# Optimization experiments

Hardware: AMD Instinct MI355X
Metric: run time of the kernel (lower is better)

Reference implementation:

```python
import jax, jax.numpy as jnp
import numpy as np

D_MODEL = 1024
N_HEADS = 16
D_HEAD = D_MODEL // N_HEADS  # 64
D_FF = D_MODEL  # FeedForward(d_model, d_model) in source
B, S = 4, 1024
EPS = 1e-5


def layer_norm(x, gamma, beta):
    mu = jnp.mean(x, axis=-1, keepdims=True)
    var = jnp.mean(jnp.square(x - mu), axis=-1, keepdims=True)
    return (x - mu) * jax.lax.rsqrt(var + EPS) * gamma + beta


def setup_inputs() -> dict:
    key = jax.random.key(0)
    ks = jax.random.split(key, 16)
    s_embed = 1.0 / np.sqrt(D_MODEL)
    s_ff = 1.0 / np.sqrt(D_FF)
    return {
        "x": jax.random.normal(ks[0], (B, S, D_MODEL), jnp.float32),
        # per-head QKV projections stacked over heads: [H, d_embed, d_head]
        "Wq": jax.random.normal(ks[1], (N_HEADS, D_MODEL, D_HEAD), jnp.float32) * s_embed,
        "bq": jax.random.normal(ks[2], (N_HEADS, D_HEAD), jnp.float32) * s_embed,
        "Wk": jax.random.normal(ks[3], (N_HEADS, D_MODEL, D_HEAD), jnp.float32) * s_embed,
        "bk": jax.random.normal(ks[4], (N_HEADS, D_HEAD), jnp.float32) * s_embed,
        "Wv": jax.random.normal(ks[5], (N_HEADS, D_MODEL, D_HEAD), jnp.float32) * s_embed,
        "bv": jax.random.normal(ks[6], (N_HEADS, D_HEAD), jnp.float32) * s_embed,
        "Wo": jax.random.normal(ks[7], (D_MODEL, D_MODEL), jnp.float32) * s_embed,
        "bo": jax.random.normal(ks[8], (D_MODEL,), jnp.float32) * s_embed,
        "g1": jnp.ones((D_MODEL,), jnp.float32),
        "be1": jnp.zeros((D_MODEL,), jnp.float32),
        "W1": jax.random.normal(ks[9], (D_MODEL, D_FF), jnp.float32) * s_embed,
        "b1": jax.random.normal(ks[10], (D_FF,), jnp.float32) * s_embed,
        "W2": jax.random.normal(ks[11], (D_FF, D_MODEL), jnp.float32) * s_ff,
        "b2": jax.random.normal(ks[12], (D_MODEL,), jnp.float32) * s_ff,
        "g2": jnp.ones((D_MODEL,), jnp.float32),
        "be2": jnp.zeros((D_MODEL,), jnp.float32),
    }


def reference(x, Wq, bq, Wk, bk, Wv, bv, Wo, bo, g1, be1, W1, b1, W2, b2, g2, be2):
    scale = 1.0 / np.sqrt(D_HEAD).astype(np.float32)
    # batched per-head projections (equivalent to the per-head Linear loop)
    Q = jnp.einsum('bse,hed->bhsd', x, Wq) + bq[None, :, None, :]
    K = jnp.einsum('bse,hed->bhsd', x, Wk) + bk[None, :, None, :]
    V = jnp.einsum('bse,hed->bhsd', x, Wv) + bv[None, :, None, :]
    scores = jnp.einsum('bhsd,bhtd->bhst', Q, K) * scale
    attn = jax.nn.softmax(scores, axis=-1)
    ctx = jnp.einsum('bhst,bhtd->bhsd', attn, V)
    # concat heads along feature dim (head order matches the torch cat)
    ctx = jnp.transpose(ctx, (0, 2, 1, 3)).reshape(x.shape[0], x.shape[1], D_MODEL)
    attn_out = ctx @ Wo + bo
    y1 = layer_norm(x + attn_out, g1, be1)
    ff = jax.nn.relu(y1 @ W1 + b1) @ W2 + b2  # dropout is identity in eval
    return layer_norm(y1 + ff, g2, be2)
```

## Files before the change

kernel.cpp:

```cpp
#include <hip/hip_runtime.h>
#include <stdint.h>

#define BSZ 4
#define SEQ 1024
#define DM 1024
#define NH 16
#define DH 64
#define ROWS (BSZ * SEQ)
#define QS3 3072

typedef unsigned short u16;
typedef short bf16x8 __attribute__((ext_vector_type(8)));
typedef float f32x4 __attribute__((ext_vector_type(4)));

__device__ __forceinline__ float b2f(u16 u) {
    union { uint32_t i; float f; } v; v.i = ((uint32_t)u) << 16; return v.f;
}
__device__ __forceinline__ u16 f2b(float f) {
    union { float f; uint32_t i; } v; v.f = f;
    uint32_t u = v.i;
    return (u16)((u + 0x7FFFu + ((u >> 16) & 1u)) >> 16);
}
__device__ __forceinline__ u16 f2b_rh(float f) {
    union { float f; uint32_t i; } v; v.f = f;
    return (u16)((v.i + 0x8000u) >> 16);
}

typedef const __attribute__((address_space(1))) void gv_t;
typedef __attribute__((address_space(3))) void lv_t;
__device__ __forceinline__ void gl_lds16(const void* g, void* l) {
    __builtin_amdgcn_global_load_lds((gv_t*)g, (lv_t*)l, 16, 0, 0);
}

__global__ __launch_bounds__(256) void detect_dtype(
    const uint32_t* __restrict__ x, int* __restrict__ flag)
{
    __shared__ int red[256];
    const int tid = threadIdx.x;
    int sane = 0;
    for (int i = tid; i < 1024; i += 256) {
        uint32_t w = x[i];
        uint32_t lo = w & 0xFFFFu;
        uint32_t e = (lo >> 7) & 0xFF;
        if ((e >= 100 && e <= 140) || lo == 0) sane++;
    }
    red[tid] = sane;
    __syncthreads();
    for (int st = 128; st > 0; st >>= 1) {
        if (tid < st) red[tid] += red[tid + st];
        __syncthreads();
    }
    if (tid == 0) flag[0] = (red[0] < 512) ? 1 : 0;
}

__global__ __launch_bounds__(256) void convert_generic(
    const void* __restrict__ src, u16* __restrict__ dst, int n,
    const int* __restrict__ flag)
{
    int i = blockIdx.x * 256 + threadIdx.x;
    if (i >= n) return;
    if (flag[0]) dst[i] = f2b(((const float*)src)[i]);
    else         dst[i] = ((const u16*)src)[i];
}

__global__ __launch_bounds__(256) void convert_vecs(
    const void* bq, const void* bk, const void* bv, const void* bo,
    const void* b1, const void* b2, const void* g1, const void* be1,
    const void* g2, const void* be2, u16* __restrict__ dst,
    const int* __restrict__ flag)
{
    int i = blockIdx.x * 256 + threadIdx.x;
    int seg = i >> 10, off = i & 1023;
    const void* srcs[10] = {bq, bk, bv, bo, b1, b2, g1, be1, g2, be2};
    const void* s = srcs[seg];
    if (flag[0]) dst[i] = f2b(((const float*)s)[off]);
    else         dst[i] = ((const u16*)s)[off];
}

__global__ __launch_bounds__(256) void transpose_convert(
    const void* __restrict__ src, u16* __restrict__ dst, int R, int C,
    const int* __restrict__ flag)
{
    __shared__ u16 Ts[32][33];
    const int t = threadIdx.x;
    const int cb = blockIdx.x * 32, rb = blockIdx.y * 32, z = blockIdx.z;
    const int tr = t >> 3, tc4 = (t & 7) * 4;
    const size_t sbase = (size_t)z * R * C;

    u16 v[4];
    if (flag[0]) {
        const float* s = (const float*)src + sbase + (size_t)(rb + tr) * C + cb + tc4;
        float4 f = *(const float4*)s;
        v[0] = f2b(f.x); v[1] = f2b(f.y); v[2] = f2b(f.z); v[3] = f2b(f.w);
    } else {
        const u16* s = (const u16*)src + sbase + (size_t)(rb + tr) * C + cb + tc4;
        ushort4 f = *(const ushort4*)s;
        v[0] = f.x; v[1] = f.y; v[2] = f.z; v[3] = f.w;
    }
    #pragma unroll
    for (int j = 0; j < 4; ++j) Ts[tc4 + j][tr] = v[j];
    __syncthreads();

    u16* d = dst + (size_t)(z * C + cb + tr) * R + rb + tc4;
    ushort4 o;
    o.x = Ts[tr][tc4 + 0]; o.y = Ts[tr][tc4 + 1];
    o.z = Ts[tr][tc4 + 2]; o.w = Ts[tr][tc4 + 3];
    *(ushort4*)d = o;
}

__global__ __launch_bounds__(256) void gemm_mfma(
    const u16* __restrict__ A, const u16* __restrict__ Bt,
    const u16* __restrict__ bias, const u16* __restrict__ resid,
    u16* __restrict__ C, int M, int N, int K, int relu)
{
    __shared__ u16 As[2][128 * 32];
    __shared__ u16 Bs[2][128 * 32];
    const int tid = threadIdx.x;
    const int w = tid >> 6, lane = tid & 63;
    const int l16 = lane & 15, quad = lane >> 4;
    const int wr = w >> 1, wc = w & 1;
    const int bm = blockIdx.y * 128, bn = blockIdx.x * 128;

    f32x4 acc[4][4];
    #pragma unroll
    for (int i = 0; i < 4; ++i)
        #pragma unroll
        for (int j = 0; j < 4; ++j)
            acc[i][j] = (f32x4){0.f, 0.f, 0.f, 0.f};

    const int srow = lane >> 2, scol = (lane & 3) * 8;
    const u16* gA0 = A  + (size_t)(bm + w * 16 + srow) * K + scol;
    const u16* gA1 = gA0 + (size_t)64 * K;
    const u16* gB0 = Bt + (size_t)(bn + w * 16 + srow) * K + scol;
    const u16* gB1 = gB0 + (size_t)64 * K;
    const int lo0 = (w * 16) * 32, lo1 = (64 + w * 16) * 32;

    gl_lds16(gA0, &As[0][lo0]);
    gl_lds16(gA1, &As[0][lo1]);
    gl_lds16(gB0, &Bs[0][lo0]);
    gl_lds16(gB1, &Bs[0][lo1]);
    __syncthreads();

    const int nk = K >> 5;
    for (int kt = 0; kt < nk; ++kt) {
        const int cur = kt & 1, nxt = cur ^ 1;
        if (kt + 1 < nk) {
            const int off = (kt + 1) * 32;
            gl_lds16(gA0 + off, &As[nxt][lo0]);
            gl_lds16(gA1 + off, &As[nxt][lo1]);
            gl_lds16(gB0 + off, &Bs[nxt][lo0]);
            gl_lds16(gB1 + off, &Bs[nxt][lo1]);
        }

        bf16x8 a[4], b[4];
        #pragma unroll
        for (int i = 0; i < 4; ++i)
            a[i] = *(const bf16x8*)&As[cur][(wr * 64 + i * 16 + l16) * 32 + quad * 8];
        #pragma unroll
        for (int j = 0; j < 4; ++j)
            b[j] = *(const bf16x8*)&Bs[cur][(wc * 64 + j * 16 + l16) * 32 + quad * 8];

        #pragma unroll
        for (int i = 0; i < 4; ++i)
            #pragma unroll
            for (int j = 0; j < 4; ++j)
                acc[i][j] = __builtin_amdgcn_mfma_f32_16x16x32_bf16(a[i], b[j], acc[i][j], 0, 0, 0);
        __syncthreads();
    }

    #pragma unroll
    for (int j = 0; j < 4; ++j) {
        const int col = bn + wc * 64 + j * 16 + l16;
        const float bj = bias ? b2f(bias[col]) : 0.f;
        #pragma unroll
        for (int i = 0; i < 4; ++i) {
            const int row0 = bm + wr * 64 + i * 16 + quad * 4;
            #pragma unroll
            for (int r = 0; r < 4; ++r) {
                const int row = row0 + r;
                float v = acc[i][j][r] + bj;
                if (resid) v += b2f(resid[(size_t)row * N + col]);
                if (relu)  v = v > 0.f ? v : 0.f;
                C[(size_t)row * N + col] = f2b(v);
            }
        }
    }
}

__global__ __launch_bounds__(256) void gemm_mfma64(
    const u16* __restrict__ A, const u16* __restrict__ Bt,
    const u16* __restrict__ bias, const u16* __restrict__ resid,
    u16* __restrict__ C, int M, int N, int K, int relu)
{
    __shared__ u16 As[2][128 * 32];
    __shared__ u16 Bs[2][64 * 32];
    const int tid = threadIdx.x;
    const int w = tid >> 6, lane = tid & 63;
    const int l16 = lane & 15, quad = lane >> 4;
    const int bm = blockIdx.y * 128, bn = blockIdx.x * 64;

    f32x4 acc[2][4];
    #pragma unroll
    for (int i = 0; i < 2; ++i)
        #pragma unroll
        for (int j = 0; j < 4; ++j)
            acc[i][j] = (f32x4){0.f, 0.f, 0.f, 0.f};

    const int srow = lane >> 2, scol = (lane & 3) * 8;
    const u16* gA0 = A  + (size_t)(bm + w * 16 + srow) * K + scol;
    const u16* gA1 = gA0 + (size_t)64 * K;
    const u16* gB0 = Bt + (size_t)(bn + w * 16 + srow) * K + scol;
    const int lo0 = (w * 16) * 32, lo1 = (64 + w * 16) * 32;

    gl_lds16(gA0, &As[0][lo0]);
    gl_lds16(gA1, &As[0][lo1]);
    gl_lds16(gB0, &Bs[0][lo0]);
    __syncthreads();

    const int nk = K >> 5;
    for (int kt = 0; kt < nk; ++kt) {
        const int cur = kt & 1, nxt = cur ^ 1;
        if (kt + 1 < nk) {
            const int off = (kt + 1) * 32;
            gl_lds16(gA0 + off, &As[nxt][lo0]);
            gl_lds16(gA1 + off, &As[nxt][lo1]);
            gl_lds16(gB0 + off, &Bs[nxt][lo0]);
        }

        bf16x8 a[2], b[4];
        #pragma unroll
        for (int i = 0; i < 2; ++i)
            a[i] = *(const bf16x8*)&As[cur][(w * 32 + i * 16 + l16) * 32 + quad * 8];
        #pragma unroll
        for (int j = 0; j < 4; ++j)
            b[j] = *(const bf16x8*)&Bs[cur][(j * 16 + l16) * 32 + quad * 8];

        #pragma unroll
        for (int i = 0; i < 2; ++i)
            #pragma unroll
            for (int j = 0; j < 4; ++j)
                acc[i][j] = __builtin_amdgcn_mfma_f32_16x16x32_bf16(a[i], b[j], acc[i][j], 0, 0, 0);
        __syncthreads();
    }

    #pragma unroll
    for (int j = 0; j < 4; ++j) {
        const int col = bn + j * 16 + l16;
        const float bj = bias ? b2f(bias[col]) : 0.f;
        #pragma unroll
        for (int i = 0; i < 2; ++i) {
            const int row0 = bm + w * 32 + i * 16 + quad * 4;
            #pragma unroll
            for (int r = 0; r < 4; ++r) {
                const int row = row0 + r;
                float v = acc[i][j][r] + bj;
                if (resid) v += b2f(resid[(size_t)row * N + col]);
                if (relu)  v = v > 0.f ? v : 0.f;
                C[(size_t)row * N + col] = f2b(v);
            }
        }
    }
}

__global__ __launch_bounds__(512) void attn_mfma(
    const u16* __restrict__ QKV, u16* __restrict__ ctx)
{
    __shared__ u16 Qf[8192];
    __shared__ u16 Kf[2][4096];
    __shared__ u16 VtT[2][64 * 72];
    __shared__ u16 Ps[8 * 16 * 72];

    const int qt = blockIdx.x, h = blockIdx.y, b = blockIdx.z;
    const int tid = threadIdx.x;
    const int w = tid >> 6, lane = tid & 63;
    const int l16 = lane & 15, quad = lane >> 4;
    const size_t qrow0 = (size_t)(b * SEQ + qt * 128);
    const size_t brow = (size_t)(b * SEQ);
    const int hoff = h * DH;

    const size_t qg = (qrow0 + w * 16 + l16) * QS3 + hoff + quad * 8;
    gl_lds16(&QKV[qg],      &Qf[w * 1024]);
    gl_lds16(&QKV[qg + 32], &Qf[w * 1024 + 512]);

    const int kt_ = w >> 1, kh_ = w & 1;
    const size_t kgbase = (size_t)(kt_ * 16 + l16) * QS3 + 1024 + hoff + kh_ * 32 + quad * 8;
    const int kdst = kt_ * 1024 + kh_ * 512;

    const int vk2 = (tid & 31) * 2, vd0 = (tid >> 5) * 4;
    const size_t vgbase = (size_t)vk2 * QS3 + 2048 + hoff + vd0;

    gl_lds16(&QKV[brow * QS3 + kgbase], &Kf[0][kdst]);
    {
        uint2 a0 = *(const uint2*)&QKV[brow * QS3 + vgbase];
        uint2 a1 = *(const uint2*)&QKV[brow * QS3 + vgbase + QS3];
        uint32_t w0 = (a0.x & 0xFFFFu) | (a1.x << 16);
        uint32_t w1 = (a0.x >> 16)     | (a1.x & 0xFFFF0000u);
        uint32_t w2 = (a0.y & 0xFFFFu) | (a1.y << 16);
        uint32_t w3 = (a0.y >> 16)     | (a1.y & 0xFFFF0000u);
        *(uint32_t*)&VtT[0][(vd0 + 0) * 72 + vk2] = w0;
        *(uint32_t*)&VtT[0][(vd0 + 1) * 72 + vk2] = w1;
        *(uint32_t*)&VtT[0][(vd0 + 2) * 72 + vk2] = w2;
        *(uint32_t*)&VtT[0][(vd0 + 3) * 72 + vk2] = w3;
    }
    __syncthreads();

    bf16x8 aQ0 = *(const bf16x8*)&Qf[w * 1024 +       lane * 8];
    bf16x8 aQ1 = *(const bf16x8*)&Qf[w * 1024 + 512 + lane * 8];

    f32x4 O[4];
    #pragma unroll
    for (int dt = 0; dt < 4; ++dt) O[dt] = (f32x4){0.f, 0.f, 0.f, 0.f};
    float lacc[4] = {0.f, 0.f, 0.f, 0.f};

    for (int kt64 = 0; kt64 < SEQ / 64; ++kt64) {
        const int cur = kt64 & 1, nxt = cur ^ 1;
        uint2 a0, a1;
        const bool more = (kt64 + 1 < SEQ / 64);
        if (more) {
            const size_t krow = brow + (size_t)(kt64 + 1) * 64;
            gl_lds16(&QKV[krow * QS3 + kgbase], &Kf[nxt][kdst]);
            a0 = *(const uint2*)&QKV[krow * QS3 + vgbase];
            a1 = *(const uint2*)&QKV[krow * QS3 + vgbase + QS3];
        }

        f32x4 St[4];
        #pragma unroll
        for (int t = 0; t < 4; ++t) {
            bf16x8 b0 = *(const bf16x8*)&Kf[cur][t * 1024 +       lane * 8];
            bf16x8 b1 = *(const bf16x8*)&Kf[cur][t * 1024 + 512 + lane * 8];
            f32x4 z = (f32x4){0.f, 0.f, 0.f, 0.f};
            z = __builtin_amdgcn_mfma_f32_16x16x32_bf16(aQ0, b0, z, 0, 0, 0);
            z = __builtin_amdgcn_mfma_f32_16x16x32_bf16(aQ1, b1, z, 0, 0, 0);
            St[t] = z;
        }

        #pragma unroll
        for (int t = 0; t < 4; ++t)
            #pragma unroll
            for (int r = 0; r < 4; ++r) {
                const float p = __expf(St[t][r] * 0.125f);
                lacc[r] += p;
                Ps[w * 1152 + (quad * 4 + r) * 72 + t * 16 + l16] = f2b_rh(p);
            }

        bf16x8 aP0 = *(const bf16x8*)&Ps[w * 1152 + l16 * 72 +  0 + quad * 8];
        bf16x8 aP1 = *(const bf16x8*)&Ps[w * 1152 + l16 * 72 + 32 + quad * 8];
        #pragma unroll
        for (int dt = 0; dt < 4; ++dt) {
            bf16x8 vv0 = *(const bf16x8*)&VtT[cur][(dt * 16 + l16) * 72 +  0 + quad * 8];
            bf16x8 vv1 = *(const bf16x8*)&VtT[cur][(dt * 16 + l16) * 72 + 32 + quad * 8];
            O[dt] = __builtin_amdgcn_mfma_f32_16x16x32_bf16(aP0, vv0, O[dt], 0, 0, 0);
            O[dt] = __builtin_amdgcn_mfma_f32_16x16x32_bf16(aP1, vv1, O[dt], 0, 0, 0);
        }

        if (more) {
            uint32_t w0 = (a0.x & 0xFFFFu) | (a1.x << 16);
            uint32_t w1 = (a0.x >> 16)     | (a1.x & 0xFFFF0000u);
            uint32_t w2 = (a0.y & 0xFFFFu) | (a1.y << 16);
            uint32_t w3 = (a0.y >> 16)     | (a1.y & 0xFFFF0000u);
            *(uint32_t*)&VtT[nxt][(vd0 + 0) * 72 + vk2] = w0;
            *(uint32_t*)&VtT[nxt][(vd0 + 1) * 72 + vk2] = w1;
            *(uint32_t*)&VtT[nxt][(vd0 + 2) * 72 + vk2] = w2;
            *(uint32_t*)&VtT[nxt][(vd0 + 3) * 72 + vk2] = w3;
        }
        __syncthreads();
    }

    #pragma unroll
    for (int r = 0; r < 4; ++r) {
        float s = lacc[r];
        s += __shfl_xor(s, 1);
        s += __shfl_xor(s, 2);
        s += __shfl_xor(s, 4);
        s += __shfl_xor(s, 8);
        const float inv = 1.0f / s;
        const size_t qgr = qrow0 + w * 16 + quad * 4 + r;
        #pragma unroll
        for (int dt = 0; dt < 4; ++dt)
            ctx[qgr * DM + hoff + dt * 16 + l16] = f2b(O[dt][r] * inv);
    }
}

__global__ __launch_bounds__(256) void layernorm_kernel(
    const u16* __restrict__ X, const u16* __restrict__ gamma,
    const u16* __restrict__ beta, void* __restrict__ Y,
    const int* __restrict__ flag, int out_adaptive)
{
    __shared__ float red[256], red2[256];
    const int r = blockIdx.x, tid = threadIdx.x;
    const u16* xp = X + (size_t)r * DM;

    ushort4 v = *(const ushort4*)(xp + tid * 4);
    float x0 = b2f(v.x), x1 = b2f(v.y), x2 = b2f(v.z), x3 = b2f(v.w);
    red[tid]  = x0 + x1 + x2 + x3;
    red2[tid] = x0 * x0 + x1 * x1 + x2 * x2 + x3 * x3;
    __syncthreads();
    for (int st = 128; st > 0; st >>= 1) {
        if (tid < st) { red[tid] += red[tid + st]; red2[tid] += red2[tid + st]; }
        __syncthreads();
    }
    const float mu = red[0] * (1.0f / DM);
    const float var = red2[0] * (1.0f / DM) - mu * mu;
    const float rstd = rsqrtf(var + 1e-5f);

    ushort4 g = *(const ushort4*)(gamma + tid * 4);
    ushort4 be = *(const ushort4*)(beta + tid * 4);
    float y0 = (x0 - mu) * rstd * b2f(g.x) + b2f(be.x);
    float y1 = (x1 - mu) * rstd * b2f(g.y) + b2f(be.y);
    float y2 = (x2 - mu) * rstd * b2f(g.z) + b2f(be.z);
    float y3 = (x3 - mu) * rstd * b2f(g.w) + b2f(be.w);

    const size_t off = (size_t)r * DM + tid * 4;
    if (out_adaptive && flag[0]) {
        float* yp = (float*)Y + off;
        yp[0] = y0; yp[1] = y1; yp[2] = y2; yp[3] = y3;
    } else {
        u16* yp = (u16*)Y + off;
        yp[0] = f2b(y0); yp[1] = f2b(y1); yp[2] = f2b(y2); yp[3] = f2b(y3);
    }
}

extern "C" void kernel_launch(void* const* d_in, const int* in_sizes, int n_in,
                              void* d_out, int out_size, void* d_ws, size_t ws_size,
                              hipStream_t stream) {
    const void* x_raw   = d_in[0];
    const void* Wq_raw  = d_in[1];
    const void* bq_raw  = d_in[2];
    const void* Wk_raw  = d_in[3];
    const void* bk_raw  = d_in[4];
    const void* Wv_raw  = d_in[5];
    const void* bv_raw  = d_in[6];
    const void* Wo_raw  = d_in[7];
    const void* bo_raw  = d_in[8];
    const void* g1_raw  = d_in[9];
    const void* be1_raw = d_in[10];
    const void* W1_raw  = d_in[11];
    const void* b1_raw  = d_in[12];
    const void* W2_raw  = d_in[13];
    const void* b2_raw  = d_in[14];
    const void* g2_raw  = d_in[15];
    const void* be2_raw = d_in[16];

    char* ws = (char*)d_ws;
    const size_t MB = 1024 * 1024;
    int* flag   = (int*)ws;
    u16* x_c    = (u16*)(ws + 1 * MB);
    u16* WqkvT  = (u16*)(ws + 9 * MB);
    u16* WoT    = (u16*)(ws + 15 * MB);
    u16* W1T    = (u16*)(ws + 17 * MB);
    u16* W2T    = (u16*)(ws + 19 * MB);
    u16* vecs   = (u16*)(ws + 21 * MB);
    u16* bqkv_c = vecs;
    u16* bo_c   = vecs + 3072;
    u16* b1_c   = vecs + 4096;
    u16* b2_c   = vecs + 5120;
    u16* g1_c   = vecs + 6144;
    u16* be1_c  = vecs + 7168;
    u16* g2_c   = vecs + 8192;
    u16* be2_c  = vecs + 9216;
    u16* QKVb   = (u16*)(ws + 22 * MB);
    u16* ctx    = (u16*)(ws + 48 * MB);
    u16* res1   = (u16*)(ws + 56 * MB);
    u16* y1     = QKVb;
    u16* hmid   = QKVb + 4 * MB;
    u16* res2   = res1;

    detect_dtype<<<1, 256, 0, stream>>>((const uint32_t*)x_raw, flag);

    const int NX = ROWS * DM;
    convert_generic<<<NX / 256, 256, 0, stream>>>(x_raw, x_c, NX, flag);

    dim3 gt_qkv(DH / 32, DM / 32, NH);
    transpose_convert<<<gt_qkv, 256, 0, stream>>>(Wq_raw, WqkvT,               DM, DH, flag);
    transpose_convert<<<gt_qkv, 256, 0, stream>>>(Wk_raw, WqkvT + 1024 * 1024, DM, DH, flag);
    transpose_convert<<<gt_qkv, 256, 0, stream>>>(Wv_raw, WqkvT + 2048 * 1024, DM, DH, flag);
    dim3 gt_sq(DM / 32, DM / 32, 1);
    transpose_convert<<<gt_sq, 256, 0, stream>>>(Wo_raw, WoT, DM, DM, flag);
    transpose_convert<<<gt_sq, 256, 0, stream>>>(W1_raw, W1T, DM, DM, flag);
    transpose_convert<<<gt_sq, 256, 0, stream>>>(W2_raw, W2T, DM, DM, flag);

    convert_vecs<<<40, 256, 0, stream>>>(bq_raw, bk_raw, bv_raw, bo_raw,
                                         b1_raw, b2_raw, g1_raw, be1_raw,
                                         g2_raw, be2_raw, vecs, flag);

    gemm_mfma<<<dim3(QS3 / 128, ROWS / 128), 256, 0, stream>>>(
        x_c, WqkvT, bqkv_c, nullptr, QKVb, ROWS, QS3, DM, 0);

    attn_mfma<<<dim3(SEQ / 128, NH, BSZ), 512, 0, stream>>>(QKVb, ctx);

    dim3 gg64(DM / 64, ROWS / 128);
    gemm_mfma64<<<gg64, 256, 0, stream>>>(ctx, WoT, bo_c, x_c, res1, ROWS, DM, DM, 0);
    layernorm_kernel<<<ROWS, 256, 0, stream>>>(res1, g1_c, be1_c, (void*)y1, flag, 0);
    gemm_mfma64<<<gg64, 256, 0, stream>>>(y1, W1T, b1_c, nullptr, hmid, ROWS, DM, DM, 1);
    gemm_mfma64<<<gg64, 256, 0, stream>>>(hmid, W2T, b2_c, y1, res2, ROWS, DM, DM, 0);
    layernorm_kernel<<<ROWS, 256, 0, stream>>>(res2, g2_c, be2_c, d_out, flag, 1);
}
```

Baseline: 303.4 us.

## Store GEMM operands in pre-tiled blocked layout and stage epilogue through LDS

Introduces a blocked tile layout (128 rows x 32 k per 4096-element tile, arranged in the MFMA fragment order) for x, the transposed weights, ctx, y1 and hmid. Every producer kernel (conversion, transpose, attention, layernorm, GEMM epilogue) now writes into this layout, so the GEMM's global-to-LDS loads become fully contiguous and its LDS reads avoid bank conflicts. GEMM epilogues also stage results in LDS and write them out as 16-byte vector stores instead of scattered 2-byte stores. The cost is more complex indexing throughout, a residual read that gathers from the blocked layout, and extra LDS traffic in the epilogue.

```diff
diff --git a/kernel.cpp b/kernel.cpp
--- a/kernel.cpp
+++ b/kernel.cpp
@@ -24,6 +24,12 @@
 __device__ __forceinline__ u16 f2b_rh(float f) {
     union { float f; uint32_t i; } v; v.f = f;
     return (u16)((v.i + 0x8000u) >> 16);
+}
+
+__device__ __forceinline__ size_t blk_idx(int row, int col, int nkt) {
+    return (((size_t)((row >> 7) * nkt + (col >> 5))) << 12)
+         + ((((row >> 4) & 7) * 64 + ((col >> 3) & 3) * 16 + (row & 15)) << 3)
+         + (col & 7);
 }
 
 typedef const __attribute__((address_space(1))) void gv_t;
@@ -53,16 +59,6 @@
     if (tid == 0) flag[0] = (red[0] < 512) ? 1 : 0;
 }
 
-__global__ __launch_bounds__(256) void convert_generic(
-    const void* __restrict__ src, u16* __restrict__ dst, int n,
-    const int* __restrict__ flag)
-{
-    int i = blockIdx.x * 256 + threadIdx.x;
-    if (i >= n) return;
-    if (flag[0]) dst[i] = f2b(((const float*)src)[i]);
-    else         dst[i] = ((const u16*)src)[i];
-}
-
 __global__ __launch_bounds__(256) void convert_vecs(
     const void* bq, const void* bk, const void* bv, const void* bo,
     const void* b1, const void* b2, const void* g1, const void* be1,
@@ -77,14 +73,36 @@
     else         dst[i] = ((const u16*)s)[off];
 }
 
-__global__ __launch_bounds__(256) void transpose_convert(
+__global__ __launch_bounds__(256) void convert_x_blocked(
+    const void* __restrict__ src, u16* __restrict__ dst,
+    const int* __restrict__ flag)
+{
+    const int gid = blockIdx.x * 256 + threadIdx.x;
+    const int tile = gid >> 9, c = gid & 511;
+    const int p = tile >> 5, t = tile & 31;
+    const int r = p * 128 + ((c >> 6) & 7) * 16 + (c & 15);
+    const int k = t * 32 + ((c >> 4) & 3) * 8;
+    union { uint4 q; u16 s[8]; } o;
+    if (flag[0]) {
+        const float* s = (const float*)src + (size_t)r * DM + k;
+        float4 f0 = *(const float4*)s;
+        float4 f1 = *(const float4*)(s + 4);
+        o.s[0] = f2b(f0.x); o.s[1] = f2b(f0.y); o.s[2] = f2b(f0.z); o.s[3] = f2b(f0.w);
+        o.s[4] = f2b(f1.x); o.s[5] = f2b(f1.y); o.s[6] = f2b(f1.z); o.s[7] = f2b(f1.w);
+    } else {
+        o.q = *(const uint4*)((const u16*)src + (size_t)r * DM + k);
+    }
+    *(uint4*)&dst[(size_t)gid * 8] = o.q;
+}
+
+__global__ __launch_bounds__(256) void transpose_blocked(
     const void* __restrict__ src, u16* __restrict__ dst, int R, int C,
-    const int* __restrict__ flag)
+    int n_off, const int* __restrict__ flag)
 {
     __shared__ u16 Ts[32][33];
-    const int t = threadIdx.x;
+    const int tid = threadIdx.x;
     const int cb = blockIdx.x * 32, rb = blockIdx.y * 32, z = blockIdx.z;
-    const int tr = t >> 3, tc4 = (t & 7) * 4;
+    const int tr = tid >> 3, tc4 = (tid & 7) * 4;
     const size_t sbase = (size_t)z * R * C;
 
     u16 v[4];
@@ -101,25 +119,37 @@
     for (int j = 0; j < 4; ++j) Ts[tc4 + j][tr] = v[j];
     __syncthreads();
 
-    u16* d = dst + (size_t)(z * C + cb + tr) * R + rb + tc4;
-    ushort4 o;
-    o.x = Ts[tr][tc4 + 0]; o.y = Ts[tr][tc4 + 1];
-    o.z = Ts[tr][tc4 + 2]; o.w = Ts[tr][tc4 + 3];
-    *(ushort4*)d = o;
-}
-
-__global__ __launch_bounds__(256) void gemm_mfma(
-    const u16* __restrict__ A, const u16* __restrict__ Bt,
+    if (tid < 128) {
+        const int np = tid & 31, qp = tid >> 5;
+        const int n = n_off + z * C + cb + np;
+        const int k = rb + qp * 8;
+        union { uint4 q; u16 s[8]; } o;
+        #pragma unroll
+        for (int j = 0; j < 8; ++j) o.s[j] = Ts[np][qp * 8 + j];
+        *(uint4*)&dst[blk_idx(n, k, 32)] = o.q;
+    }
+}
+
+__global__ __launch_bounds__(256) void gemm_b128(
+    const u16* __restrict__ Ab, const u16* __restrict__ Bb,
     const u16* __restrict__ bias, const u16* __restrict__ resid,
-    u16* __restrict__ C, int M, int N, int K, int relu)
-{
-    __shared__ u16 As[2][128 * 32];
-    __shared__ u16 Bs[2][128 * 32];
+    u16* __restrict__ C, int M, int N, int K,
+    int relu, int c_blocked, int resid_blocked)
+{
+    __shared__ uint4 smem4[2176];
+    u16* As = (u16*)smem4;
+    u16* Bs = (u16*)smem4 + 8192;
+    u16* Cs = (u16*)smem4;
+
     const int tid = threadIdx.x;
     const int w = tid >> 6, lane = tid & 63;
     const int l16 = lane & 15, quad = lane >> 4;
     const int wr = w >> 1, wc = w & 1;
     const int bm = blockIdx.y * 128, bn = blockIdx.x * 128;
+    const int nkt = K >> 5;
+
+    const u16* At = Ab + ((size_t)(bm >> 7) * nkt << 12);
+    const u16* Bt = Bb + ((size_t)(bn >> 7) * nkt << 12);
 
     f32x4 acc[4][4];
     #pragma unroll
@@ -128,37 +158,31 @@
         for (int j = 0; j < 4; ++j)
             acc[i][j] = (f32x4){0.f, 0.f, 0.f, 0.f};
 
-    const int srow = lane >> 2, scol = (lane & 3) * 8;
-    const u16* gA0 = A  + (size_t)(bm + w * 16 + srow) * K + scol;
-    const u16* gA1 = gA0 + (size_t)64 * K;
-    const u16* gB0 = Bt + (size_t)(bn + w * 16 + srow) * K + scol;
-    const u16* gB1 = gB0 + (size_t)64 * K;
-    const int lo0 = (w * 16) * 32, lo1 = (64 + w * 16) * 32;
-
-    gl_lds16(gA0, &As[0][lo0]);
-    gl_lds16(gA1, &As[0][lo1]);
-    gl_lds16(gB0, &Bs[0][lo0]);
-    gl_lds16(gB1, &Bs[0][lo1]);
-    __syncthreads();
-
-    const int nk = K >> 5;
-    for (int kt = 0; kt < nk; ++kt) {
-        const int cur = kt & 1, nxt = cur ^ 1;
-        if (kt + 1 < nk) {
-            const int off = (kt + 1) * 32;
-            gl_lds16(gA0 + off, &As[nxt][lo0]);
-            gl_lds16(gA1 + off, &As[nxt][lo1]);
-            gl_lds16(gB0 + off, &Bs[nxt][lo0]);
-            gl_lds16(gB1 + off, &Bs[nxt][lo1]);
+    const int co0 = (w * 64) * 8, co1 = (256 + w * 64) * 8;
+
+    gl_lds16(&At[(size_t)0 + (w * 64 + lane) * 8],         &As[co0]);
+    gl_lds16(&At[(size_t)0 + (256 + w * 64 + lane) * 8],   &As[co1]);
+    gl_lds16(&Bt[(size_t)0 + (w * 64 + lane) * 8],         &Bs[co0]);
+    gl_lds16(&Bt[(size_t)0 + (256 + w * 64 + lane) * 8],   &Bs[co1]);
+    __syncthreads();
+
+    for (int kt = 0; kt < nkt; ++kt) {
+        const int cur = (kt & 1) * 4096, nxt = cur ^ 4096;
+        if (kt + 1 < nkt) {
+            const size_t tb = (size_t)(kt + 1) << 12;
+            gl_lds16(&At[tb + (w * 64 + lane) * 8],       &As[nxt + co0]);
+            gl_lds16(&At[tb + (256 + w * 64 + lane) * 8], &As[nxt + co1]);
+            gl_lds16(&Bt[tb + (w * 64 + lane) * 8],       &Bs[nxt + co0]);
+            gl_lds16(&Bt[tb + (256 + w * 64 + lane) * 8], &Bs[nxt + co1]);
         }
 
         bf16x8 a[4], b[4];
         #pragma unroll
         for (int i = 0; i < 4; ++i)
-            a[i] = *(const bf16x8*)&As[cur][(wr * 64 + i * 16 + l16) * 32 + quad * 8];
+            a[i] = *(const bf16x8*)&As[cur + (((wr * 4 + i) * 64) + quad * 16 + l16) * 8];
         #pragma unroll
         for (int j = 0; j < 4; ++j)
-            b[j] = *(const bf16x8*)&Bs[cur][(wc * 64 + j * 16 + l16) * 32 + quad * 8];
+            b[j] = *(const bf16x8*)&Bs[cur + (((wc * 4 + j) * 64) + quad * 16 + l16) * 8];
 
         #pragma unroll
         for (int i = 0; i < 4; ++i)
@@ -170,34 +194,69 @@
 
     #pragma unroll
     for (int j = 0; j < 4; ++j) {
-        const int col = bn + wc * 64 + j * 16 + l16;
+        const int lc = wc * 64 + j * 16 + l16;
+        const int col = bn + lc;
         const float bj = bias ? b2f(bias[col]) : 0.f;
         #pragma unroll
         for (int i = 0; i < 4; ++i) {
-            const int row0 = bm + wr * 64 + i * 16 + quad * 4;
             #pragma unroll
             for (int r = 0; r < 4; ++r) {
-                const int row = row0 + r;
+                const int lr = wr * 64 + i * 16 + quad * 4 + r;
                 float v = acc[i][j][r] + bj;
-                if (resid) v += b2f(resid[(size_t)row * N + col]);
-                if (relu)  v = v > 0.f ? v : 0.f;
-                C[(size_t)row * N + col] = f2b(v);
+                if (resid) {
+                    const size_t ri = resid_blocked ? blk_idx(bm + lr, col, N >> 5)
+                                                    : (size_t)(bm + lr) * N + col;
+                    v += b2f(resid[ri]);
+                }
+                if (relu) v = v > 0.f ? v : 0.f;
+                Cs[lr * 136 + lc] = f2b(v);
             }
         }
     }
-}
-
-__global__ __launch_bounds__(256) void gemm_mfma64(
-    const u16* __restrict__ A, const u16* __restrict__ Bt,
+    __syncthreads();
+
+    if (!c_blocked) {
+        #pragma unroll
+        for (int u = 0; u < 8; ++u) {
+            const int g = u * 256 + tid;
+            const int row = g >> 4, c16 = g & 15;
+            uint4 val = *(const uint4*)&Cs[row * 136 + c16 * 8];
+            *(uint4*)&C[(size_t)(bm + row) * N + bn + c16 * 8] = val;
+        }
+    } else {
+        const size_t obase = ((size_t)((bm >> 7) * (N >> 5) + (bn >> 5))) << 12;
+        #pragma unroll
+        for (int u = 0; u < 8; ++u) {
+            const int cc = u * 256 + tid;
+            const int t2 = cc >> 9, c = cc & 511;
+            const int row = ((c >> 6) & 7) * 16 + (c & 15);
+            const int col = t2 * 32 + ((c >> 4) & 3) * 8;
+            uint4 val = *(const uint4*)&Cs[row * 136 + col];
+            *(uint4*)&C[obase + ((size_t)t2 << 12) + (size_t)c * 8] = val;
+        }
+    }
+}
+
+__global__ __launch_bounds__(256) void gemm_b64(
+    const u16* __restrict__ Ab, const u16* __restrict__ Bb,
     const u16* __restrict__ bias, const u16* __restrict__ resid,
-    u16* __restrict__ C, int M, int N, int K, int relu)
-{
-    __shared__ u16 As[2][128 * 32];
-    __shared__ u16 Bs[2][64 * 32];
+    u16* __restrict__ C, int M, int N, int K,
+    int relu, int c_blocked, int resid_blocked)
+{
+    __shared__ uint4 smem4[1536];
+    u16* As = (u16*)smem4;
+    u16* Bs = (u16*)smem4 + 8192;
+    u16* Cs = (u16*)smem4;
+
     const int tid = threadIdx.x;
     const int w = tid >> 6, lane = tid & 63;
     const int l16 = lane & 15, quad = lane >> 4;
     const int bm = blockIdx.y * 128, bn = blockIdx.x * 64;
+    const int nkt = K >> 5;
+
+    const u16* At = Ab + ((size_t)(bm >> 7) * nkt << 12);
+    const int bsub = ((bn >> 6) & 1) * 256;
+    const u16* Bt = Bb + ((size_t)(bn >> 7) * nkt << 12);
 
     f32x4 acc[2][4];
     #pragma unroll
@@ -206,34 +265,30 @@
         for (int j = 0; j < 4; ++j)
             acc[i][j] = (f32x4){0.f, 0.f, 0.f, 0.f};
 
-    const int srow = lane >> 2, scol = (lane & 3) * 8;
-    const u16* gA0 = A  + (size_t)(bm + w * 16 + srow) * K + scol;
-    const u16* gA1 = gA0 + (size_t)64 * K;
-    const u16* gB0 = Bt + (size_t)(bn + w * 16 + srow) * K + scol;
-    const int lo0 = (w * 16) * 32, lo1 = (64 + w * 16) * 32;
-
-    gl_lds16(gA0, &As[0][lo0]);
-    gl_lds16(gA1, &As[0][lo1]);
-    gl_lds16(gB0, &Bs[0][lo0]);
-    __syncthreads();
-
-    const int nk = K >> 5;
-    for (int kt = 0; kt < nk; ++kt) {
-        const int cur = kt & 1, nxt = cur ^ 1;
-        if (kt + 1 < nk) {
-            const int off = (kt + 1) * 32;
-            gl_lds16(gA0 + off, &As[nxt][lo0]);
-            gl_lds16(gA1 + off, &As[nxt][lo1]);
-            gl_lds16(gB0 + off, &Bs[nxt][lo0]);
+    const int co0 = (w * 64) * 8, co1 = (256 + w * 64) * 8;
+
+    gl_lds16(&At[(size_t)0 + (w * 64 + lane) * 8],       &As[co0]);
+    gl_lds16(&At[(size_t)0 + (256 + w * 64 + lane) * 8], &As[co1]);
+    gl_lds16(&Bt[(size_t)0 + (bsub + w * 64 + lane) * 8], &Bs[co0]);
+    __syncthreads();
+
+    for (int kt = 0; kt < nkt; ++kt) {
+        const int curA = (kt & 1) * 4096, nxtA = curA ^ 4096;
+        const int curB = (kt & 1) * 2048, nxtB = curB ^ 2048;
+        if (kt + 1 < nkt) {
+            const size_t tb = (size_t)(kt + 1) << 12;
+            gl_lds16(&At[tb + (w * 64 + lane) * 8],        &As[nxtA + co0]);
+            gl_lds16(&At[tb + (256 + w * 64 + lane) * 8],  &As[nxtA + co1]);
+            gl_lds16(&Bt[tb + (bsub + w * 64 + lane) * 8], &Bs[nxtB + co0]);
         }
 
         bf16x8 a[2], b[4];
         #pragma unroll
         for (int i = 0; i < 2; ++i)
-            a[i] = *(const bf16x8*)&As[cur][(w * 32 + i * 16 + l16) * 32 + quad * 8];
+            a[i] = *(const bf16x8*)&As[curA + (((w * 2 + i) * 64) + quad * 16 + l16) * 8];
         #pragma unroll
         for (int j = 0; j < 4; ++j)
-            b[j] = *(const bf16x8*)&Bs[cur][(j * 16 + l16) * 32 + quad * 8];
+            b[j] = *(const bf16x8*)&Bs[curB + ((j * 64) + quad * 16 + l16) * 8];
 
         #pragma unroll
         for (int i = 0; i < 2; ++i)
@@ -245,19 +300,45 @@
 
     #pragma unroll
     for (int j = 0; j < 4; ++j) {
-        const int col = bn + j * 16 + l16;
+        const int lc = j * 16 + l16;
+        const int col = bn + lc;
         const float bj = bias ? b2f(bias[col]) : 0.f;
         #pragma unroll
         for (int i = 0; i < 2; ++i) {
-            const int row0 = bm + w * 32 + i * 16 + quad * 4;
             #pragma unroll
             for (int r = 0; r < 4; ++r) {
-                const int row = row0 + r;
+                const int lr = w * 32 + i * 16 + quad * 4 + r;
                 float v = acc[i][j][r] + bj;
-                if (resid) v += b2f(resid[(size_t)row * N + col]);
-                if (relu)  v = v > 0.f ? v : 0.f;
-                C[(size_t)row * N + col] = f2b(v);
+                if (resid) {
+                    const size_t ri = resid_blocked ? blk_idx(bm + lr, col, N >> 5)
+                                                    : (size_t)(bm + lr) * N + col;
+                    v += b2f(resid[ri]);
+                }
+                if (relu) v = v > 0.f ? v : 0.f;
+                Cs[lr * 72 + lc] = f2b(v);
             }
+        }
+    }
+    __syncthreads();
+
+    if (!c_blocked) {
+        #pragma unroll
+        for (int u = 0; u < 4; ++u) {
+            const int g = u * 256 + tid;
+            const int row = g >> 3, c16 = g & 7;
+            uint4 val = *(const uint4*)&Cs[row * 72 + c16 * 8];
+            *(uint4*)&C[(size_t)(bm + row) * N + bn + c16 * 8] = val;
+        }
+    } else {
+        const size_t obase = ((size_t)((bm >> 7) * (N >> 5) + (bn >> 5))) << 12;
+        #pragma unroll
+        for (int u = 0; u < 4; ++u) {
+            const int cc = u * 256 + tid;
+            const int t2 = cc >> 9, c = cc & 511;
+            const int row = ((c >> 6) & 7) * 16 + (c & 15);
+            const int col = t2 * 32 + ((c >> 4) & 3) * 8;
+            uint4 val = *(const uint4*)&Cs[row * 72 + col];
+            *(uint4*)&C[obase + ((size_t)t2 << 12) + (size_t)c * 8] = val;
         }
     }
 }
@@ -366,6 +447,7 @@
         __syncthreads();
     }
 
+    const size_t pbase = ((size_t)(qrow0 >> 7) * 32) << 12;
     #pragma unroll
     for (int r = 0; r < 4; ++r) {
         float s = lacc[r];
@@ -374,17 +456,21 @@
         s += __shfl_xor(s, 4);
         s += __shfl_xor(s, 8);
         const float inv = 1.0f / s;
-        const size_t qgr = qrow0 + w * 16 + quad * 4 + r;
-        #pragma unroll
-        for (int dt = 0; dt < 4; ++dt)
-            ctx[qgr * DM + hoff + dt * 16 + l16] = f2b(O[dt][r] * inv);
+        #pragma unroll
+        for (int dt = 0; dt < 4; ++dt) {
+            const int t = h * 2 + (dt >> 1);
+            const int q = (dt & 1) * 2 + (l16 >> 3);
+            const size_t idx = pbase + ((size_t)t << 12)
+                             + ((w * 64 + q * 16 + quad * 4 + r) << 3) + (l16 & 7);
+            ctx[idx] = f2b(O[dt][r] * inv);
+        }
     }
 }
 
 __global__ __launch_bounds__(256) void layernorm_kernel(
     const u16* __restrict__ X, const u16* __restrict__ gamma,
     const u16* __restrict__ beta, void* __restrict__ Y,
-    const int* __restrict__ flag, int out_adaptive)
+    const int* __restrict__ flag, int y_mode)
 {
     __shared__ float red[256], red2[256];
     const int r = blockIdx.x, tid = threadIdx.x;
@@ -410,13 +496,18 @@
     float y2 = (x2 - mu) * rstd * b2f(g.z) + b2f(be.z);
     float y3 = (x3 - mu) * rstd * b2f(g.w) + b2f(be.w);
 
-    const size_t off = (size_t)r * DM + tid * 4;
-    if (out_adaptive && flag[0]) {
-        float* yp = (float*)Y + off;
+    const int k = tid * 4;
+    if (y_mode == 2 && flag[0]) {
+        float* yp = (float*)Y + (size_t)r * DM + k;
         yp[0] = y0; yp[1] = y1; yp[2] = y2; yp[3] = y3;
+    } else if (y_mode == 1) {
+        u16* yp = (u16*)Y + blk_idx(r, k, 32);
+        ushort4 o; o.x = f2b(y0); o.y = f2b(y1); o.z = f2b(y2); o.w = f2b(y3);
+        *(ushort4*)yp = o;
     } else {
-        u16* yp = (u16*)Y + off;
-        yp[0] = f2b(y0); yp[1] = f2b(y1); yp[2] = f2b(y2); yp[3] = f2b(y3);
+        u16* yp = (u16*)Y + (size_t)r * DM + k;
+        ushort4 o; o.x = f2b(y0); o.y = f2b(y1); o.z = f2b(y2); o.w = f2b(y3);
+        *(ushort4*)yp = o;
     }
 }
 
@@ -444,11 +535,11 @@
     char* ws = (char*)d_ws;
     const size_t MB = 1024 * 1024;
     int* flag   = (int*)ws;
-    u16* x_c    = (u16*)(ws + 1 * MB);
-    u16* WqkvT  = (u16*)(ws + 9 * MB);
-    u16* WoT    = (u16*)(ws + 15 * MB);
-    u16* W1T    = (u16*)(ws + 17 * MB);
-    u16* W2T    = (u16*)(ws + 19 * MB);
+    u16* x_b    = (u16*)(ws + 1 * MB);
+    u16* WqkvB  = (u16*)(ws + 9 * MB);
+    u16* WoB    = (u16*)(ws + 15 * MB);
+    u16* W1B    = (u16*)(ws + 17 * MB);
+    u16* W2B    = (u16*)(ws + 19 * MB);
     u16* vecs   = (u16*)(ws + 21 * MB);
     u16* bqkv_c = vecs;
     u16* bo_c   = vecs + 3072;
@@ -459,39 +550,38 @@
     u16* g2_c   = vecs + 8192;
     u16* be2_c  = vecs + 9216;
     u16* QKVb   = (u16*)(ws + 22 * MB);
-    u16* ctx    = (u16*)(ws + 48 * MB);
+    u16* y1B    = QKVb;
+    u16* hmidB  = QKVb + 4 * MB;
+    u16* ctxB   = (u16*)(ws + 48 * MB);
     u16* res1   = (u16*)(ws + 56 * MB);
-    u16* y1     = QKVb;
-    u16* hmid   = QKVb + 4 * MB;
     u16* res2   = res1;
 
     detect_dtype<<<1, 256, 0, stream>>>((const uint32_t*)x_raw, flag);
 
-    const int NX = ROWS * DM;
-    convert_generic<<<NX / 256, 256, 0, stream>>>(x_raw, x_c, NX, flag);
-
-    dim3 gt_qkv(DH / 32, DM / 32, NH);
-    transpose_convert<<<gt_qkv, 256, 0, stream>>>(Wq_raw, WqkvT,               DM, DH, flag);
-    transpose_convert<<<gt_qkv, 256, 0, stream>>>(Wk_raw, WqkvT + 1024 * 1024, DM, DH, flag);
-    transpose_convert<<<gt_qkv, 256, 0, stream>>>(Wv_raw, WqkvT + 2048 * 1024, DM, DH, flag);
-    dim3 gt_sq(DM / 32, DM / 32, 1);
-    transpose_convert<<<gt_sq, 256, 0, stream>>>(Wo_raw, WoT, DM, DM, flag);
-    transpose_convert<<<gt_sq, 256, 0, stream>>>(W1_raw, W1T, DM, DM, flag);
-    transpose_convert<<<gt_sq, 256, 0, stream>>>(W2_raw, W2T, DM, DM, flag);
+    convert_x_blocked<<<2048, 256, 0, stream>>>(x_raw, x_b, flag);
+
+    dim3 gt_qkv(2, 32, NH);
+    transpose_blocked<<<gt_qkv, 256, 0, stream>>>(Wq_raw, WqkvB, DM, DH,    0, flag);
+    transpose_blocked<<<gt_qkv, 256, 0, stream>>>(Wk_raw, WqkvB, DM, DH, 1024, flag);
+    transpose_blocked<<<gt_qkv, 256, 0, stream>>>(Wv_raw, WqkvB, DM, DH, 2048, flag);
+    dim3 gt_sq(32, 32, 1);
+    transpose_blocked<<<gt_sq, 256, 0, stream>>>(Wo_raw, WoB, DM, DM, 0, flag);
+    transpose_blocked<<<gt_sq, 256, 0, stream>>>(W1_raw, W1B, DM, DM, 0, flag);
+    transpose_blocked<<<gt_sq, 256, 0, stream>>>(W2_raw, W2B, DM, DM, 0, flag);
 
     convert_vecs<<<40, 256, 0, stream>>>(bq_raw, bk_raw, bv_raw, bo_raw,
                                          b1_raw, b2_raw, g1_raw, be1_raw,
                                          g2_raw, be2_raw, vecs, flag);
 
-    gemm_mfma<<<dim3(QS3 / 128, ROWS / 128), 256, 0, stream>>>(
-        x_c, WqkvT, bqkv_c, nullptr, QKVb, ROWS, QS3, DM, 0);
-
-    attn_mfma<<<dim3(SEQ / 128, NH, BSZ), 512, 0, stream>>>(QKVb, ctx);
+    gemm_b128<<<dim3(QS3 / 128, ROWS / 128), 256, 0, stream>>>(
+        x_b, WqkvB, bqkv_c, nullptr, QKVb, ROWS, QS3, DM, 0, 0, 0);
+
+    attn_mfma<<<dim3(SEQ / 128, NH, BSZ), 512, 0, stream>>>(QKVb, ctxB);
 
     dim3 gg64(DM / 64, ROWS / 128);
-    gemm_mfma64<<<gg64, 256, 0, stream>>>(ctx, WoT, bo_c, x_c, res1, ROWS, DM, DM, 0);
-    layernorm_kernel<<<ROWS, 256, 0, stream>>>(res1, g1_c, be1_c, (void*)y1, flag, 0);
-    gemm_mfma64<<<gg64, 256, 0, stream>>>(y1, W1T, b1_c, nullptr, hmid, ROWS, DM, DM, 1);
-    gemm_mfma64<<<gg64, 256, 0, stream>>>(hmid, W2T, b2_c, y1, res2, ROWS, DM, DM, 0);
-    layernorm_kernel<<<ROWS, 256, 0, stream>>>(res2, g2_c, be2_c, d_out, flag, 1);
-}
+    gemm_b64<<<gg64, 256, 0, stream>>>(ctxB, WoB, bo_c, x_b, res1, ROWS, DM, DM, 0, 0, 1);
+    layernorm_kernel<<<ROWS, 256, 0, stream>>>(res1, g1_c, be1_c, (void*)y1B, flag, 1);
+    gemm_b64<<<gg64, 256, 0, stream>>>(y1B, W1B, b1_c, nullptr, hmidB, ROWS, DM, DM, 1, 1, 0);
+    gemm_b64<<<gg64, 256, 0, stream>>>(hmidB, W2B, b2_c, y1B, res2, ROWS, DM, DM, 0, 0, 1);
+    layernorm_kernel<<<ROWS, 256, 0, stream>>>(res2, g2_c, be2_c, d_out, flag, 2);
+}
```

New measurement: 277.5 us. 1.09x faster.
